# Optimization experiments

Measured on AMD Instinct MI355X. Metric: run time of the kernel, lower is better.

## Reference

```python
import jax, jax.numpy as jnp
import numpy as np
import math

DIM = 1024
NUM_HEADS = 16
HEAD_DIM = DIM // NUM_HEADS


def build_rope_matrix(dim, seq_len):
    # (seq_len, dim): concat of cos(freqs) and sin(freqs), each (seq_len, dim//2)
    position = jnp.arange(seq_len, dtype=jnp.float32)[:, None]
    dim_pair = jnp.arange(0, dim, 2, dtype=jnp.float32)[None, :]
    theta = 10000.0 ** (-dim_pair / dim)
    freqs = position * theta  # (seq_len, dim//2)
    return jnp.concatenate([jnp.cos(freqs), jnp.sin(freqs)], axis=-1)


def apply_rope(x, rope):
    # x: (..., N, d), rope: (N, d). Faithful to the torch code's strided slicing.
    x1, x2 = x[..., ::2], x[..., 1::2]
    cos = rope[..., ::2]
    sin = rope[..., 1::2]
    return jnp.concatenate([x1 * cos - x2 * sin, x1 * sin + x2 * cos], axis=-1)


def setup_inputs() -> dict:
    key = jax.random.key(0)
    ks = jax.random.split(key, 9)
    B, N = 2, 2048
    x = jax.random.normal(ks[0], (B, N, DIM), dtype=jnp.float32)
    # Xavier-uniform-ish linear weights (dim, dim), zero-mean biases
    bound = math.sqrt(6.0 / (DIM + DIM))
    def w(k):
        return jax.random.uniform(k, (DIM, DIM), jnp.float32, -bound, bound)
    def b(k):
        return jax.random.uniform(k, (DIM,), jnp.float32, -1.0 / math.sqrt(DIM), 1.0 / math.sqrt(DIM))
    return {
        "x": x,
        "Wq": w(ks[1]), "bq": b(ks[2]),
        "Wk": w(ks[3]), "bk": b(ks[4]),
        "Wv": w(ks[5]), "bv": b(ks[6]),
        "Wo": w(ks[7]), "bo": b(ks[8]),
    }


def reference(x, Wq, bq, Wk, bk, Wv, bv, Wo, bo):
    B, N, _ = x.shape
    H, hd = NUM_HEADS, HEAD_DIM
    rope = build_rope_matrix(hd, N)  # (N, hd)

    def proj(W, bias):
        y = x @ W.T + bias               # (B, N, dim)
        return y.reshape(B, N, H, hd).transpose(0, 2, 1, 3)  # (B, H, N, hd)

    q = apply_rope(proj(Wq, bq), rope)
    k = apply_rope(proj(Wk, bk), rope)
    v = apply_rope(proj(Wv, bv), rope)

    scores = jnp.einsum("bhqd,bhkd->bhqk", q, k) / math.sqrt(hd)
    probs = jax.nn.softmax(scores, axis=-1)
    out = jnp.einsum("bhqk,bhkd->bhqd", probs, v)  # (B, H, N, hd)

    out = apply_rope(out, -rope)  # inverse RoPE (as defined: negate rope)
    out = out.transpose(0, 2, 1, 3).reshape(B, N, DIM)
    return out @ Wo.T + bo
```

## Files before the change

kernel.cpp:

```cpp
#include <hip/hip_runtime.h>
#include <hip/hip_bf16.h>
#include <math.h>

#define NHEADS 16
#define HDIM   64
#define BATCH  2
#define SEQLEN 2048
#define DIMSZ  1024

typedef _Float16 f16x8 __attribute__((ext_vector_type(8)));
typedef float    f32x4 __attribute__((ext_vector_type(4)));
typedef unsigned short u16x8 __attribute__((ext_vector_type(8)));
typedef unsigned int   u32x4 __attribute__((ext_vector_type(4)));

__device__ __forceinline__ float rope_theta(int c) {
    int i = c & 31;
    return (float)pow(10000.0, -(double)i / 32.0);
}
__device__ __forceinline__ unsigned short f16u(float f) {
    _Float16 h = (_Float16)f;
    return *reinterpret_cast<unsigned short*>(&h);
}
__device__ __forceinline__ void async_copy16(const void* gsrc, void* lds) {
    __builtin_amdgcn_global_load_lds(
        (const __attribute__((address_space(1))) unsigned int*)gsrc,
        (__attribute__((address_space(3))) unsigned int*)lds, 16, 0, 0);
}

__global__ __launch_bounds__(256) void prep_kernel(
    const float* __restrict__ x, const float* __restrict__ Wq,
    const float* __restrict__ Wk, const float* __restrict__ Wv,
    const float* __restrict__ Wo, const float* __restrict__ bq,
    const float* __restrict__ bk, const float* __restrict__ bv,
    unsigned short* __restrict__ x16, unsigned short* __restrict__ Wqkv16,
    unsigned short* __restrict__ Wo16, float* __restrict__ biasqkv,
    float* __restrict__ ropeC, float* __restrict__ ropeS)
{
    const int NV = (4194304 + 4 * 1048576) / 8;
    int gid = blockIdx.x * 256 + threadIdx.x;
    for (int i = gid; i < NV; i += gridDim.x * 256) {
        long e = (long)i * 8;
        const float* src; unsigned short* dst; long off;
        if (e < 4194304)      { src = x;  dst = x16;              off = e; }
        else if (e < 5242880) { src = Wq; dst = Wqkv16;           off = e - 4194304; }
        else if (e < 6291456) { src = Wk; dst = Wqkv16 + 1048576; off = e - 5242880; }
        else if (e < 7340032) { src = Wv; dst = Wqkv16 + 2097152; off = e - 6291456; }
        else                  { src = Wo; dst = Wo16;             off = e - 7340032; }
        float4 v0 = *reinterpret_cast<const float4*>(src + off);
        float4 v1 = *reinterpret_cast<const float4*>(src + off + 4);
        u16x8 o;
        o[0] = f16u(v0.x); o[1] = f16u(v0.y); o[2] = f16u(v0.z); o[3] = f16u(v0.w);
        o[4] = f16u(v1.x); o[5] = f16u(v1.y); o[6] = f16u(v1.z); o[7] = f16u(v1.w);
        *reinterpret_cast<u16x8*>(dst + off) = o;
    }
    if (gid < 65536) {
        int npos = gid >> 5, j = gid & 31;
        float f = (float)npos * rope_theta(j);
        ropeC[gid] = cosf(f);
        ropeS[gid] = sinf(f);
    }
    if (gid < 3072) {
        biasqkv[gid] = gid < 1024 ? bq[gid] : (gid < 2048 ? bk[gid - 1024] : bv[gid - 2048]);
    }
}

__global__ __launch_bounds__(512, 4) void qkv_gemm_kernel(
    const unsigned short* __restrict__ A, const unsigned short* __restrict__ B,
    const float* __restrict__ bias, const float* __restrict__ ropeC,
    const float* __restrict__ ropeS, unsigned short* __restrict__ QKV)
{
    __shared__ __align__(16) unsigned char smem[65536];
    const int tid = threadIdx.x;
    const int w = tid >> 6, l = tid & 63;
    const int g = l >> 4, lx = l & 15;
    const int wr = w >> 2, wc = w & 3;
    const int row0 = blockIdx.y * 128;
    const int col0 = blockIdx.x * 128;
    const unsigned short* Ab = A + (size_t)row0 * DIMSZ;
    const unsigned short* Bb = B + (size_t)col0 * DIMSZ;

    const int sr = tid >> 3;
    const int sc = tid & 7;
    const int ssw = sc ^ (sr & 7);
    const size_t sAoff0 = (size_t)sr * DIMSZ + ssw * 8;
    const size_t sAoff1 = (size_t)(64 + sr) * DIMSZ + ssw * 8;

    f32x4 acc[4][2] = {};
    async_copy16(Ab + sAoff0, smem + tid * 16);
    async_copy16(Ab + sAoff1, smem + 8192 + tid * 16);
    async_copy16(Bb + sAoff0, smem + 16384 + tid * 16);
    async_copy16(Bb + sAoff1, smem + 16384 + 8192 + tid * 16);
    __syncthreads();

    int buf = 0;
    for (int k0 = 0; k0 < DIMSZ; k0 += 64) {
        if (k0 + 64 < DIMSZ) {
            const int nb = (buf ^ 1) * 32768;
            async_copy16(Ab + sAoff0 + k0 + 64, smem + nb + tid * 16);
            async_copy16(Ab + sAoff1 + k0 + 64, smem + nb + 8192 + tid * 16);
            async_copy16(Bb + sAoff0 + k0 + 64, smem + nb + 16384 + tid * 16);
            async_copy16(Bb + sAoff1 + k0 + 64, smem + nb + 16384 + 8192 + tid * 16);
        }
        const int ab = buf * 32768, bb2 = ab + 16384;
        #pragma unroll
        for (int ks = 0; ks < 2; ++ks) {
            f16x8 af[4], bf[2];
            #pragma unroll
            for (int m = 0; m < 4; ++m) {
                int r = wr * 64 + m * 16 + lx;
                af[m] = *reinterpret_cast<const f16x8*>(
                    &smem[ab + r * 128 + ((ks * 64 + g * 16) ^ ((r & 7) << 4))]);
            }
            #pragma unroll
            for (int n = 0; n < 2; ++n) {
                int r = wc * 32 + n * 16 + lx;
                bf[n] = *reinterpret_cast<const f16x8*>(
                    &smem[bb2 + r * 128 + ((ks * 64 + g * 16) ^ ((r & 7) << 4))]);
            }
            #pragma unroll
            for (int m = 0; m < 4; ++m)
                #pragma unroll
                for (int n = 0; n < 2; ++n)
                    acc[m][n] = __builtin_amdgcn_mfma_f32_16x16x32_f16(af[m], bf[n], acc[m][n], 0, 0, 0);
        }
        __syncthreads();
        buf ^= 1;
    }

    const int proj = col0 >> 10;
    const int cin128 = (col0 & 1023);
    float bsv[2];
    #pragma unroll
    for (int n = 0; n < 2; ++n) bsv[n] = bias[col0 + wc * 32 + n * 16 + lx];

    if (proj == 2) {
        _Float16* T = (_Float16*)smem;
        #pragma unroll
        for (int m = 0; m < 4; ++m) {
            int rl0 = wr * 64 + m * 16 + g * 4;
            #pragma unroll
            for (int r2 = 0; r2 < 4; ++r2) {
                int rlocal = rl0 + r2;
                int npos = (row0 + rlocal) & (SEQLEN - 1);
                const float* rcp = ropeC + npos * 32;
                const float* rsp = ropeS + npos * 32;
                #pragma unroll
                for (int n = 0; n < 2; ++n) {
                    float v = acc[m][n][r2] + bsv[n];
                    float o = __shfl_xor(v, 1);
                    int dcol = wc * 32 + n * 16 + lx;
                    int c = dcol & 63;
                    const float* tab = (c < 32) ? rcp : rsp;
                    float Rd = tab[c & 31];
                    float Rp = tab[(c & 31) ^ 1];
                    float y; int outc;
                    if (c & 1) { y = o * Rd + v * Rp; outc = (c >> 1) + 32; }
                    else       { y = v * Rd - o * Rp; outc = c >> 1; }
                    T[((dcol >> 6) * 64 + outc) * 136 + rlocal] = (_Float16)y;
                }
            }
        }
        __syncthreads();
        int b = row0 >> 11, npos0 = row0 & (SEQLEN - 1);
        int hd0 = cin128 >> 6;
        int trow = tid >> 2;
        int cbase = (tid & 3) * 32;
        int head = hd0 + (trow >> 6);
        int outd = trow & 63;
        unsigned short* vdst = QKV + 8388608 +
            (((size_t)b * NHEADS + head) * HDIM + outd) * SEQLEN + npos0 + cbase;
        #pragma unroll
        for (int i2 = 0; i2 < 4; ++i2) {
            f16x8 val = *reinterpret_cast<const f16x8*>(&T[trow * 136 + cbase + i2 * 8]);
            *reinterpret_cast<f16x8*>(vdst + i2 * 8) = val;
        }
    } else {
        #pragma unroll
        for (int m = 0; m < 4; ++m) {
            int rbase = row0 + wr * 64 + m * 16 + g * 4;
            #pragma unroll
            for (int r2 = 0; r2 < 4; ++r2) {
                int rglob = rbase + r2;
                int b = rglob >> 11, npos = rglob & (SEQLEN - 1);
                const float* rcp = ropeC + npos * 32;
                const float* rsp = ropeS + npos * 32;
                #pragma unroll
                for (int n = 0; n < 2; ++n) {
                    float v = acc[m][n][r2] + bsv[n];
                    float o = __shfl_xor(v, 1);
                    int hd = (cin128 + wc * 32 + n * 16) >> 6;
                    int c = ((wc * 32 + n * 16) & 63) + lx;
                    const float* tab = (c < 32) ? rcp : rsp;
                    float Rd = tab[c & 31];
                    float Rp = tab[(c & 31) ^ 1];
                    float y; int outc;
                    if (c & 1) { y = o * Rd + v * Rp; outc = (c >> 1) + 32; }
                    else       { y = v * Rd - o * Rp; outc = c >> 1; }
                    unsigned short* Orow = QKV +
                        ((((size_t)proj * BATCH + b) * NHEADS + hd) * SEQLEN + npos) * HDIM;
                    Orow[outc] = f16u(y);
                }
            }
        }
    }
}

__global__ __launch_bounds__(512, 4) void attn_mfma_kernel(
    const unsigned short* __restrict__ QKV, const float* __restrict__ ropeC,
    const float* __restrict__ ropeS, unsigned short* __restrict__ Y)
{
    __shared__ __align__(16) unsigned char smem[36864];
    const int tid = threadIdx.x;
    const int w   = tid >> 6;
    const int l   = tid & 63;
    const int g   = l >> 4;
    const int lx  = l & 15;
    const int qg  = w & 3;
    const int kh  = w >> 2;
    const int fb  = blockIdx.x;
    const int xcd = fb & 7, jj = fb >> 3;
    const int bh  = xcd * 4 + (jj & 3);
    const int b   = bh >> 4;
    const int h   = bh & 15;
    const int q0  = (jj >> 2) * 128;

    const unsigned short* Qb  = QKV + (size_t)bh * SEQLEN * HDIM;
    const unsigned short* Kb  = QKV + 4194304 + (size_t)bh * SEQLEN * HDIM;
    const unsigned short* Vtb = QKV + 8388608 + (size_t)bh * SEQLEN * HDIM;

    f16x8 qf[2][2];
    #pragma unroll
    for (int qt = 0; qt < 2; ++qt) {
        const unsigned short* src = Qb + (size_t)(q0 + qg * 32 + qt * 16 + lx) * HDIM + g * 8;
        qf[qt][0] = *reinterpret_cast<const f16x8*>(src);
        qf[qt][1] = *reinterpret_cast<const f16x8*>(src + 32);
    }
    f16x8 ones8;
    #pragma unroll
    for (int i = 0; i < 8; ++i) ones8[i] = (_Float16)1.0f;

    const float K2 = 0.18033688011112043f;
    f32x4 oacc[2][4] = {};
    f32x4 lsum[2] = {};
    float mrow[2] = {-1e30f, -1e30f};

    const int srow = tid >> 3;
    const int c8   = tid & 7;
    const int sch  = c8 ^ (srow & 7);
    const int sdst = tid * 16;
    const int kperm = (srow & 32) + (((srow >> 2) & 3) << 3) + (((srow >> 4) & 1) << 2) + (srow & 3);
    const unsigned short* Kp = Kb + (size_t)kperm * HDIM + sch * 8;
    const unsigned short* Vp = Vtb + (size_t)srow * SEQLEN + sch * 8;

    async_copy16(Kp, smem + sdst);
    async_copy16(Vp, smem + 8192 + sdst);
    Kp += 64 * HDIM; Vp += 64;
    __syncthreads();

    const int sw = (lx & 7) << 4;
    unsigned kb0 = (kh * 32 + lx) * 128 + ((g * 16) ^ sw);
    unsigned kb1 = (kh * 32 + lx) * 128 + ((64 + g * 16) ^ sw);
    unsigned vb0 = 8192 + lx * 128 + ((kh * 64 + g * 16) ^ sw);
    unsigned nst = 16384 + sdst;

    for (int kt = 0; kt < SEQLEN / 64; ++kt) {
        if (kt + 1 < SEQLEN / 64) {
            async_copy16(Kp, smem + nst);
            async_copy16(Vp, smem + 8192 + nst);
            Kp += 64 * HDIM; Vp += 64;
        }

        f16x8 kf00 = *reinterpret_cast<const f16x8*>(&smem[kb0]);
        f16x8 kf01 = *reinterpret_cast<const f16x8*>(&smem[kb1]);
        f16x8 kf10 = *reinterpret_cast<const f16x8*>(&smem[kb0 + 2048]);
        f16x8 kf11 = *reinterpret_cast<const f16x8*>(&smem[kb1 + 2048]);

        f16x8 pfrag[2];
        #pragma unroll
        for (int qt = 0; qt < 2; ++qt) {
            f32x4 s0 = {}, s1 = {};
            __builtin_amdgcn_s_setprio(1);
            s0 = __builtin_amdgcn_mfma_f32_16x16x32_f16(kf00, qf[qt][0], s0, 0, 0, 0);
            s0 = __builtin_amdgcn_mfma_f32_16x16x32_f16(kf01, qf[qt][1], s0, 0, 0, 0);
            s1 = __builtin_amdgcn_mfma_f32_16x16x32_f16(kf10, qf[qt][0], s1, 0, 0, 0);
            s1 = __builtin_amdgcn_mfma_f32_16x16x32_f16(kf11, qf[qt][1], s1, 0, 0, 0);
            __builtin_amdgcn_s_setprio(0);

            float lmax = fmaxf(fmaxf(fmaxf(s0[0], s0[1]), fmaxf(s0[2], s0[3])),
                               fmaxf(fmaxf(s1[0], s1[1]), fmaxf(s1[2], s1[3])));
            bool ok = (lmax <= mrow[qt] + 64.f);
            if (!__all((int)ok)) {
                float m2 = fmaxf(lmax, __shfl_xor(lmax, 16));
                m2 = fmaxf(m2, __shfl_xor(m2, 32));
                float mnew = fmaxf(mrow[qt], m2);
                float sc = __builtin_amdgcn_exp2f((mrow[qt] - mnew) * K2);
                mrow[qt] = mnew;
                lsum[qt] *= sc;
                #pragma unroll
                for (int c2 = 0; c2 < 4; ++c2) oacc[qt][c2] *= sc;
            }
            float mk = -mrow[qt] * K2;
            #pragma unroll
            for (int r = 0; r < 4; ++r) {
                s0[r] = __builtin_amdgcn_exp2f(fmaf(s0[r], K2, mk));
                s1[r] = __builtin_amdgcn_exp2f(fmaf(s1[r], K2, mk));
            }
            u32x4 pw;
            pw[0] = __builtin_bit_cast(unsigned, __builtin_amdgcn_cvt_pkrtz(s0[0], s0[1]));
            pw[1] = __builtin_bit_cast(unsigned, __builtin_amdgcn_cvt_pkrtz(s0[2], s0[3]));
            pw[2] = __builtin_bit_cast(unsigned, __builtin_amdgcn_cvt_pkrtz(s1[0], s1[1]));
            pw[3] = __builtin_bit_cast(unsigned, __builtin_amdgcn_cvt_pkrtz(s1[2], s1[3]));
            pfrag[qt] = __builtin_bit_cast(f16x8, pw);
        }

        __builtin_amdgcn_s_setprio(1);
        lsum[0] = __builtin_amdgcn_mfma_f32_16x16x32_f16(ones8, pfrag[0], lsum[0], 0, 0, 0);
        lsum[1] = __builtin_amdgcn_mfma_f32_16x16x32_f16(ones8, pfrag[1], lsum[1], 0, 0, 0);
        #pragma unroll
        for (int c2 = 0; c2 < 4; ++c2) {
            f16x8 vf = *reinterpret_cast<const f16x8*>(&smem[vb0 + c2 * 2048]);
            oacc[0][c2] = __builtin_amdgcn_mfma_f32_16x16x32_f16(vf, pfrag[0], oacc[0][c2], 0, 0, 0);
            oacc[1][c2] = __builtin_amdgcn_mfma_f32_16x16x32_f16(vf, pfrag[1], oacc[1][c2], 0, 0, 0);
        }
        __builtin_amdgcn_s_setprio(0);

        __syncthreads();
        kb0 ^= 16384; kb1 ^= 16384; vb0 ^= 16384; nst ^= 16384;
    }

    if (kh == 1) {
        #pragma unroll
        for (int qt = 0; qt < 2; ++qt) {
            float* Of = (float*)smem + (qg * 2 + qt) * 1120;
            #pragma unroll
            for (int c2 = 0; c2 < 4; ++c2)
                *reinterpret_cast<f32x4*>(&Of[lx * 68 + c2 * 16 + g * 4]) = oacc[qt][c2];
            if (g == 0) {
                Of[1088 + lx] = mrow[qt];
                Of[1104 + lx] = lsum[qt][0];
            }
        }
    }
    __syncthreads();
    if (kh == 0) {
        #pragma unroll
        for (int qt = 0; qt < 2; ++qt) {
            float* Of = (float*)smem + (qg * 2 + qt) * 1120;
            float m_hi = Of[1088 + lx];
            float l_hi = Of[1104 + lx];
            float M = fmaxf(mrow[qt], m_hi);
            float a  = __builtin_amdgcn_exp2f((mrow[qt] - M) * K2);
            float bb = __builtin_amdgcn_exp2f((m_hi - M) * K2);
            float inv = 1.0f / (a * lsum[qt][0] + bb * l_hi);
            const int q = q0 + qg * 32 + qt * 16 + lx;
            unsigned short* drow = Y + ((size_t)b * SEQLEN + q) * DIMSZ + h * HDIM;
            #pragma unroll
            for (int c2 = 0; c2 < 4; ++c2) {
                f32x4 ohi = *reinterpret_cast<const f32x4*>(&Of[lx * 68 + c2 * 16 + g * 4]);
                const float* tab = ((c2 < 2) ? ropeC : ropeS) + (size_t)q * 32;
                unsigned short lo16[2], hi16[2];
                #pragma unroll
                for (int rp = 0; rp < 2; ++rp) {
                    int d = c2 * 16 + g * 4 + 2 * rp;
                    float v0 = (a * oacc[qt][c2][2 * rp]     + bb * ohi[2 * rp])     * inv;
                    float v1 = (a * oacc[qt][c2][2 * rp + 1] + bb * ohi[2 * rp + 1]) * inv;
                    float Rd = tab[d & 31], Rn = tab[(d & 31) + 1];
                    lo16[rp] = f16u(-(v0 * Rd - v1 * Rn));
                    hi16[rp] = f16u(-(v0 * Rn + v1 * Rd));
                }
                int p = c2 * 8 + g * 2;
                *reinterpret_cast<unsigned*>(&drow[p])      = (unsigned)lo16[0] | ((unsigned)lo16[1] << 16);
                *reinterpret_cast<unsigned*>(&drow[p + 32]) = (unsigned)hi16[0] | ((unsigned)hi16[1] << 16);
            }
        }
    }
}

__global__ __launch_bounds__(512, 4) void out_gemm_kernel(
    const unsigned short* __restrict__ A, const unsigned short* __restrict__ B,
    const float* __restrict__ bias, float* __restrict__ Out)
{
    __shared__ __align__(16) unsigned char smem[65536];
    const int tid = threadIdx.x;
    const int w = tid >> 6, l = tid & 63;
    const int g = l >> 4, lx = l & 15;
    const int wr = w >> 2, wc = w & 3;
    const int row0 = blockIdx.y * 128;
    const int col0 = blockIdx.x * 128;
    const unsigned short* Ab = A + (size_t)row0 * DIMSZ;
    const unsigned short* Bb = B + (size_t)col0 * DIMSZ;

    const int sr = tid >> 3;
    const int sc = tid & 7;
    const int ssw = sc ^ (sr & 7);
    const size_t sAoff0 = (size_t)sr * DIMSZ + ssw * 8;
    const size_t sAoff1 = (size_t)(64 + sr) * DIMSZ + ssw * 8;

    f32x4 acc[4][2] = {};
    async_copy16(Ab + sAoff0, smem + tid * 16);
    async_copy16(Ab + sAoff1, smem + 8192 + tid * 16);
    async_copy16(Bb + sAoff0, smem + 16384 + tid * 16);
    async_copy16(Bb + sAoff1, smem + 16384 + 8192 + tid * 16);
    __syncthreads();

    int buf = 0;
    for (int k0 = 0; k0 < DIMSZ; k0 += 64) {
        if (k0 + 64 < DIMSZ) {
            const int nb = (buf ^ 1) * 32768;
            async_copy16(Ab + sAoff0 + k0 + 64, smem + nb + tid * 16);
            async_copy16(Ab + sAoff1 + k0 + 64, smem + nb + 8192 + tid * 16);
            async_copy16(Bb + sAoff0 + k0 + 64, smem + nb + 16384 + tid * 16);
            async_copy16(Bb + sAoff1 + k0 + 64, smem + nb + 16384 + 8192 + tid * 16);
        }
        const int ab = buf * 32768, bb2 = ab + 16384;
        #pragma unroll
        for (int ks = 0; ks < 2; ++ks) {
            f16x8 af[4], bf[2];
            #pragma unroll
            for (int m = 0; m < 4; ++m) {
                int r = wr * 64 + m * 16 + lx;
                af[m] = *reinterpret_cast<const f16x8*>(
                    &smem[ab + r * 128 + ((ks * 64 + g * 16) ^ ((r & 7) << 4))]);
            }
            #pragma unroll
            for (int n = 0; n < 2; ++n) {
                int r = wc * 32 + n * 16 + lx;
                bf[n] = *reinterpret_cast<const f16x8*>(
                    &smem[bb2 + r * 128 + ((ks * 64 + g * 16) ^ ((r & 7) << 4))]);
            }
            #pragma unroll
            for (int m = 0; m < 4; ++m)
                #pragma unroll
                for (int n = 0; n < 2; ++n)
                    acc[m][n] = __builtin_amdgcn_mfma_f32_16x16x32_f16(af[m], bf[n], acc[m][n], 0, 0, 0);
        }
        __syncthreads();
        buf ^= 1;
    }

    const int cb0 = col0 + wc * 32;
    float bsv[2];
    #pragma unroll
    for (int n = 0; n < 2; ++n) bsv[n] = bias[cb0 + n * 16 + lx];
    #pragma unroll
    for (int m = 0; m < 4; ++m) {
        int rbase = row0 + wr * 64 + m * 16 + g * 4;
        #pragma unroll
        for (int r2 = 0; r2 < 4; ++r2) {
            float* orow = Out + (size_t)(rbase + r2) * DIMSZ + cb0;
            #pragma unroll
            for (int n = 0; n < 2; ++n)
                orow[n * 16 + lx] = acc[m][n][r2] + bsv[n];
        }
    }
}

extern "C" void kernel_launch(void* const* d_in, const int* in_sizes, int n_in,
                              void* d_out, int out_size, void* d_ws, size_t ws_size,
                              hipStream_t stream) {
    const float* x  = (const float*)d_in[0];
    const float* Wq = (const float*)d_in[1];
    const float* bq = (const float*)d_in[2];
    const float* Wk = (const float*)d_in[3];
    const float* bk = (const float*)d_in[4];
    const float* Wv = (const float*)d_in[5];
    const float* bv = (const float*)d_in[6];
    const float* Wo = (const float*)d_in[7];
    const float* bo = (const float*)d_in[8];
    float* out = (float*)d_out;

    char* ws = (char*)d_ws;
    unsigned short* x16    = (unsigned short*)(ws);
    unsigned short* Wqkv16 = (unsigned short*)(ws + 8388608);
    unsigned short* Wo16   = (unsigned short*)(ws + 14680064);
    float* biasqkv         = (float*)(ws + 16777216);
    float* ropeC           = (float*)(ws + 16793600);
    float* ropeS           = (float*)(ws + 17055744);
    unsigned short* QKVw   = (unsigned short*)(ws + 17825792);
    unsigned short* Yw     = (unsigned short*)(ws + 42991616);

    prep_kernel<<<dim3(2048), dim3(256), 0, stream>>>(x, Wq, Wk, Wv, Wo, bq, bk, bv,
                                                x16, Wqkv16, Wo16, biasqkv, ropeC, ropeS);
    qkv_gemm_kernel<<<dim3(24, 32), dim3(512), 0, stream>>>(x16, Wqkv16, biasqkv, ropeC, ropeS, QKVw);
    attn_mfma_kernel<<<dim3(512), dim3(512), 0, stream>>>(QKVw, ropeC, ropeS, Yw);
    out_gemm_kernel<<<dim3(8, 32), dim3(512), 0, stream>>>(Yw, Wo16, bo, out);
}
```

Measured before the change: 119.8 us.

## Double attention KV tile to 128 keys per iteration with new V swizzle

Each loop iteration of the attention kernel now stages 128 keys of K and V (64 per key-half warp group) instead of 64, halving the number of barriers and loop iterations. Shared memory grows to 64KB for the double-buffered larger tiles, and V uses a new 16-way XOR swizzle over 256-byte rows. The s_setprio hints are removed. The larger LDS footprint and extra score registers may reduce occupancy below the declared launch bound.

```diff
diff --git a/kernel.cpp b/kernel.cpp
--- a/kernel.cpp
+++ b/kernel.cpp
@@ -209,7 +209,7 @@
     const unsigned short* __restrict__ QKV, const float* __restrict__ ropeC,
     const float* __restrict__ ropeS, unsigned short* __restrict__ Y)
 {
-    __shared__ __align__(16) unsigned char smem[36864];
+    __shared__ __align__(16) unsigned char smem[65536];
     const int tid = threadIdx.x;
     const int w   = tid >> 6;
     const int l   = tid & 63;
@@ -247,47 +247,57 @@
     const int srow = tid >> 3;
     const int c8   = tid & 7;
     const int sch  = c8 ^ (srow & 7);
-    const int sdst = tid * 16;
     const int kperm = (srow & 32) + (((srow >> 2) & 3) << 3) + (((srow >> 4) & 1) << 2) + (srow & 3);
     const unsigned short* Kp = Kb + (size_t)kperm * HDIM + sch * 8;
-    const unsigned short* Vp = Vtb + (size_t)srow * SEQLEN + sch * 8;
-
-    async_copy16(Kp, smem + sdst);
-    async_copy16(Vp, smem + 8192 + sdst);
-    Kp += 64 * HDIM; Vp += 64;
+    const int vrow = tid >> 4;
+    const int vsw  = ((tid & 15) ^ (vrow & 15)) * 8;
+    const unsigned short* Vp0 = Vtb + (size_t)vrow * SEQLEN + vsw;
+    const unsigned short* Vp1 = Vtb + (size_t)(32 + vrow) * SEQLEN + vsw;
+
+    async_copy16(Kp, smem + tid * 16);
+    async_copy16(Kp + 64 * HDIM, smem + 8192 + tid * 16);
+    async_copy16(Vp0, smem + 16384 + tid * 16);
+    async_copy16(Vp1, smem + 16384 + 8192 + tid * 16);
+    Kp += 128 * HDIM; Vp0 += 128; Vp1 += 128;
     __syncthreads();
 
     const int sw = (lx & 7) << 4;
-    unsigned kb0 = (kh * 32 + lx) * 128 + ((g * 16) ^ sw);
-    unsigned kb1 = (kh * 32 + lx) * 128 + ((64 + g * 16) ^ sw);
-    unsigned vb0 = 8192 + lx * 128 + ((kh * 64 + g * 16) ^ sw);
-    unsigned nst = 16384 + sdst;
-
-    for (int kt = 0; kt < SEQLEN / 64; ++kt) {
-        if (kt + 1 < SEQLEN / 64) {
-            async_copy16(Kp, smem + nst);
-            async_copy16(Vp, smem + 8192 + nst);
-            Kp += 64 * HDIM; Vp += 64;
-        }
-
-        f16x8 kf00 = *reinterpret_cast<const f16x8*>(&smem[kb0]);
-        f16x8 kf01 = *reinterpret_cast<const f16x8*>(&smem[kb1]);
-        f16x8 kf10 = *reinterpret_cast<const f16x8*>(&smem[kb0 + 2048]);
-        f16x8 kf11 = *reinterpret_cast<const f16x8*>(&smem[kb1 + 2048]);
-
-        f16x8 pfrag[2];
+    unsigned kb0 = (kh * 64 + lx) * 128 + ((g * 16) ^ sw);
+    unsigned kb1 = (kh * 64 + lx) * 128 + ((64 + g * 16) ^ sw);
+    unsigned vbr = 16384 + lx * 256;
+    unsigned vb0 = vbr + ((kh * 128 + g * 16) ^ (lx << 4));
+    unsigned vb1 = vbr + ((kh * 128 + 64 + g * 16) ^ (lx << 4));
+    unsigned nstK = 32768 + tid * 16;
+    unsigned nstV = 32768 + 16384 + tid * 16;
+
+    for (int kt = 0; kt < 16; ++kt) {
+        if (kt < 15) {
+            async_copy16(Kp, smem + nstK);
+            async_copy16(Kp + 64 * HDIM, smem + nstK + 8192);
+            async_copy16(Vp0, smem + nstV);
+            async_copy16(Vp1, smem + nstV + 8192);
+            Kp += 128 * HDIM; Vp0 += 128; Vp1 += 128;
+        }
+
+        f32x4 s[2][4] = {};
+        #pragma unroll
+        for (int c = 0; c < 4; ++c) {
+            f16x8 kf0 = *reinterpret_cast<const f16x8*>(&smem[kb0 + c * 2048]);
+            f16x8 kf1 = *reinterpret_cast<const f16x8*>(&smem[kb1 + c * 2048]);
+            s[0][c] = __builtin_amdgcn_mfma_f32_16x16x32_f16(kf0, qf[0][0], s[0][c], 0, 0, 0);
+            s[0][c] = __builtin_amdgcn_mfma_f32_16x16x32_f16(kf1, qf[0][1], s[0][c], 0, 0, 0);
+            s[1][c] = __builtin_amdgcn_mfma_f32_16x16x32_f16(kf0, qf[1][0], s[1][c], 0, 0, 0);
+            s[1][c] = __builtin_amdgcn_mfma_f32_16x16x32_f16(kf1, qf[1][1], s[1][c], 0, 0, 0);
+        }
+
+        f16x8 pfrag[2][2];
         #pragma unroll
         for (int qt = 0; qt < 2; ++qt) {
-            f32x4 s0 = {}, s1 = {};
-            __builtin_amdgcn_s_setprio(1);
-            s0 = __builtin_amdgcn_mfma_f32_16x16x32_f16(kf00, qf[qt][0], s0, 0, 0, 0);
-            s0 = __builtin_amdgcn_mfma_f32_16x16x32_f16(kf01, qf[qt][1], s0, 0, 0, 0);
-            s1 = __builtin_amdgcn_mfma_f32_16x16x32_f16(kf10, qf[qt][0], s1, 0, 0, 0);
-            s1 = __builtin_amdgcn_mfma_f32_16x16x32_f16(kf11, qf[qt][1], s1, 0, 0, 0);
-            __builtin_amdgcn_s_setprio(0);
-
-            float lmax = fmaxf(fmaxf(fmaxf(s0[0], s0[1]), fmaxf(s0[2], s0[3])),
-                               fmaxf(fmaxf(s1[0], s1[1]), fmaxf(s1[2], s1[3])));
+            float lmax = s[qt][0][0];
+            #pragma unroll
+            for (int c = 0; c < 4; ++c)
+                #pragma unroll
+                for (int r = 0; r < 4; ++r) lmax = fmaxf(lmax, s[qt][c][r]);
             bool ok = (lmax <= mrow[qt] + 64.f);
             if (!__all((int)ok)) {
                 float m2 = fmaxf(lmax, __shfl_xor(lmax, 16));
@@ -301,31 +311,41 @@
             }
             float mk = -mrow[qt] * K2;
             #pragma unroll
-            for (int r = 0; r < 4; ++r) {
-                s0[r] = __builtin_amdgcn_exp2f(fmaf(s0[r], K2, mk));
-                s1[r] = __builtin_amdgcn_exp2f(fmaf(s1[r], K2, mk));
-            }
-            u32x4 pw;
-            pw[0] = __builtin_bit_cast(unsigned, __builtin_amdgcn_cvt_pkrtz(s0[0], s0[1]));
-            pw[1] = __builtin_bit_cast(unsigned, __builtin_amdgcn_cvt_pkrtz(s0[2], s0[3]));
-            pw[2] = __builtin_bit_cast(unsigned, __builtin_amdgcn_cvt_pkrtz(s1[0], s1[1]));
-            pw[3] = __builtin_bit_cast(unsigned, __builtin_amdgcn_cvt_pkrtz(s1[2], s1[3]));
-            pfrag[qt] = __builtin_bit_cast(f16x8, pw);
-        }
-
-        __builtin_amdgcn_s_setprio(1);
-        lsum[0] = __builtin_amdgcn_mfma_f32_16x16x32_f16(ones8, pfrag[0], lsum[0], 0, 0, 0);
-        lsum[1] = __builtin_amdgcn_mfma_f32_16x16x32_f16(ones8, pfrag[1], lsum[1], 0, 0, 0);
+            for (int c = 0; c < 4; ++c)
+                #pragma unroll
+                for (int r = 0; r < 4; ++r)
+                    s[qt][c][r] = __builtin_amdgcn_exp2f(fmaf(s[qt][c][r], K2, mk));
+            #pragma unroll
+            for (int kg = 0; kg < 2; ++kg) {
+                u32x4 pw;
+                pw[0] = __builtin_bit_cast(unsigned, __builtin_amdgcn_cvt_pkrtz(s[qt][2 * kg][0], s[qt][2 * kg][1]));
+                pw[1] = __builtin_bit_cast(unsigned, __builtin_amdgcn_cvt_pkrtz(s[qt][2 * kg][2], s[qt][2 * kg][3]));
+                pw[2] = __builtin_bit_cast(unsigned, __builtin_amdgcn_cvt_pkrtz(s[qt][2 * kg + 1][0], s[qt][2 * kg + 1][1]));
+                pw[3] = __builtin_bit_cast(unsigned, __builtin_amdgcn_cvt_pkrtz(s[qt][2 * kg + 1][2], s[qt][2 * kg + 1][3]));
+                pfrag[qt][kg] = __builtin_bit_cast(f16x8, pw);
+            }
+        }
+
+        lsum[0] = __builtin_amdgcn_mfma_f32_16x16x32_f16(ones8, pfrag[0][0], lsum[0], 0, 0, 0);
+        lsum[1] = __builtin_amdgcn_mfma_f32_16x16x32_f16(ones8, pfrag[1][0], lsum[1], 0, 0, 0);
         #pragma unroll
         for (int c2 = 0; c2 < 4; ++c2) {
-            f16x8 vf = *reinterpret_cast<const f16x8*>(&smem[vb0 + c2 * 2048]);
-            oacc[0][c2] = __builtin_amdgcn_mfma_f32_16x16x32_f16(vf, pfrag[0], oacc[0][c2], 0, 0, 0);
-            oacc[1][c2] = __builtin_amdgcn_mfma_f32_16x16x32_f16(vf, pfrag[1], oacc[1][c2], 0, 0, 0);
-        }
-        __builtin_amdgcn_s_setprio(0);
+            f16x8 vf = *reinterpret_cast<const f16x8*>(&smem[vb0 + c2 * 4096]);
+            oacc[0][c2] = __builtin_amdgcn_mfma_f32_16x16x32_f16(vf, pfrag[0][0], oacc[0][c2], 0, 0, 0);
+            oacc[1][c2] = __builtin_amdgcn_mfma_f32_16x16x32_f16(vf, pfrag[1][0], oacc[1][c2], 0, 0, 0);
+        }
+        lsum[0] = __builtin_amdgcn_mfma_f32_16x16x32_f16(ones8, pfrag[0][1], lsum[0], 0, 0, 0);
+        lsum[1] = __builtin_amdgcn_mfma_f32_16x16x32_f16(ones8, pfrag[1][1], lsum[1], 0, 0, 0);
+        #pragma unroll
+        for (int c2 = 0; c2 < 4; ++c2) {
+            f16x8 vf = *reinterpret_cast<const f16x8*>(&smem[vb1 + c2 * 4096]);
+            oacc[0][c2] = __builtin_amdgcn_mfma_f32_16x16x32_f16(vf, pfrag[0][1], oacc[0][c2], 0, 0, 0);
+            oacc[1][c2] = __builtin_amdgcn_mfma_f32_16x16x32_f16(vf, pfrag[1][1], oacc[1][c2], 0, 0, 0);
+        }
 
         __syncthreads();
-        kb0 ^= 16384; kb1 ^= 16384; vb0 ^= 16384; nst ^= 16384;
+        kb0 ^= 32768; kb1 ^= 32768; vb0 ^= 32768; vb1 ^= 32768;
+        nstK ^= 32768; nstV ^= 32768;
     }
 
     if (kh == 1) {
```

New measurement: 117.4 us. -2.0%, faster.
